# Optimization experiments

Measured on AMD Instinct MI355X. Metric: run time of the kernel, lower is better.

Reference implementation:

```python
import jax, jax.numpy as jnp
import numpy as np

N_NODES = 100000
N_EDGES = 1600000
F_IN = 128
HID = 128
LAT = 64
NUM_LAYERS = 3
NUM_GRAPHS = 512


def setup_inputs() -> dict:
    key = jax.random.key(0)
    ks = jax.random.split(key, 12)
    x = jax.random.normal(ks[0], (N_NODES, F_IN), dtype=jnp.float32)
    edge_index = jax.random.randint(ks[1], (2, N_EDGES), 0, N_NODES, dtype=jnp.int64)
    batch = jnp.sort(jax.random.randint(ks[2], (N_NODES,), 0, NUM_GRAPHS, dtype=jnp.int32))
    s_in = 1.0 / np.sqrt(F_IN)
    s_h = 1.0 / np.sqrt(HID)
    W_in = jax.random.uniform(ks[3], (F_IN, HID), jnp.float32, -s_in, s_in)
    b_in = jax.random.uniform(ks[4], (HID,), jnp.float32, -s_in, s_in)
    W_msg = jax.random.uniform(ks[5], (NUM_LAYERS, HID, HID), jnp.float32, -s_h, s_h)
    b_msg = jax.random.uniform(ks[6], (NUM_LAYERS, HID), jnp.float32, -s_h, s_h)
    W_upd = jax.random.uniform(ks[7], (NUM_LAYERS, HID, HID), jnp.float32, -s_h, s_h)
    b_upd = jax.random.uniform(ks[8], (NUM_LAYERS, HID), jnp.float32, -s_h, s_h)
    W_mean = jax.random.uniform(ks[9], (HID, LAT), jnp.float32, -s_h, s_h)
    b_mean = jax.random.uniform(ks[10], (LAT,), jnp.float32, -s_h, s_h)
    W_logvar = jax.random.uniform(ks[11], (HID, LAT), jnp.float32, -s_h, s_h)
    b_logvar = jax.random.uniform(jax.random.fold_in(key, 99), (LAT,), jnp.float32, -s_h, s_h)
    return {"x": x, "edge_index": edge_index, "batch": batch,
            "W_in": W_in, "b_in": b_in, "W_msg": W_msg, "b_msg": b_msg,
            "W_upd": W_upd, "b_upd": b_upd, "W_mean": W_mean, "b_mean": b_mean,
            "W_logvar": W_logvar, "b_logvar": b_logvar}


def _mp_layer(h, src, dst, Wm, bm, Wu, bu):
    # message: Linear+ReLU on all nodes, gather per-edge, scatter-add into dst
    messages = jax.nn.relu(h @ Wm + bm)                      # [N, H]
    agg = jax.ops.segment_sum(messages[src], dst, num_segments=N_NODES)  # [N, H]
    return jax.nn.relu(agg @ Wu + bu) + h                    # update + residual


def reference(x, edge_index, batch, W_in, b_in, W_msg, b_msg, W_upd, b_upd,
              W_mean, b_mean, W_logvar, b_logvar):
    src = edge_index[0]
    dst = edge_index[1]
    h = jax.nn.relu(x @ W_in + b_in)
    for l in range(NUM_LAYERS):
        h = _mp_layer(h, src, dst, W_msg[l], b_msg[l], W_upd[l], b_upd[l])
    # graph-level sum pooling by batch segment ids
    g = jax.ops.segment_sum(h, batch, num_segments=NUM_GRAPHS)  # [G, H]
    z_mean = g @ W_mean + b_mean
    z_logvar = g @ W_logvar + b_logvar
    return (z_mean, z_logvar)
```

## Files before the change

kernel.cpp:

```cpp
#include <hip/hip_runtime.h>
#include <hip/hip_bf16.h>
#include <cstdint>

#define N_NODES 100000
#define N_EDGES 1600000
#define N_GRAPHS 512
#define N_LAYERS 3
#define NB 1563
#define BCAP 2048
#define NFB 256

typedef __bf16 bf16x8 __attribute__((ext_vector_type(8)));
typedef float f32x4 __attribute__((ext_vector_type(4)));
typedef uint uint4v __attribute__((ext_vector_type(4)));

__device__ __forceinline__ float bf2f(ushort u) {
  uint v = ((uint)u) << 16;
  return __builtin_bit_cast(float, v);
}
__device__ __forceinline__ ushort f2bf(float f) {
  uint u = __builtin_bit_cast(uint, f);
  u += 0x7FFF + ((u >> 16) & 1);
  return (ushort)(u >> 16);
}
__device__ __forceinline__ uint pk2(float lo, float hi) {
  return (uint)f2bf(lo) | ((uint)f2bf(hi) << 16);
}

__global__ __launch_bounds__(1024) void k_bfill3(const int* __restrict__ e32,
    const long long* __restrict__ e64, int* __restrict__ bcur,
    uint* __restrict__ packed) {
  __shared__ int lcnt[NB];
  __shared__ int lbase[NB];
  __shared__ int sflag;
  const int t = threadIdx.x;
  const int e0 = blockIdx.x * (N_EDGES / NFB);
  const int e1 = e0 + (N_EDGES / NFB);
  for (int k = t; k < NB; k += 1024) lcnt[k] = 0;
  if (t == 0) {
    int any = 0;
    for (int i = 1; i < 128; i += 2) any |= e32[i];
    sflag = (any == 0) ? 1 : 0;
  }
  __syncthreads();
  const bool f64 = (sflag != 0);
  if (f64) {
    for (int i = e0 + t; i < e1; i += 1024)
      atomicAdd(&lcnt[((int)e64[N_EDGES + i]) >> 6], 1);
  } else {
    for (int i = e0 + t; i < e1; i += 1024)
      atomicAdd(&lcnt[e32[N_EDGES + i] >> 6], 1);
  }
  __syncthreads();
  for (int k = t; k < NB; k += 1024) {
    int c = lcnt[k];
    lbase[k] = (c > 0) ? atomicAdd(&bcur[k * 16], c) : 0;
    lcnt[k] = 0;
  }
  __syncthreads();
  for (int i = e0 + t; i < e1; i += 1024) {
    int d, s;
    if (f64) { d = (int)e64[N_EDGES + i]; s = (int)e64[i]; }
    else     { d = e32[N_EDGES + i];      s = e32[i]; }
    int bk = d >> 6;
    int pos = lbase[bk] + atomicAdd(&lcnt[bk], 1);
    if (pos < BCAP)
      packed[(size_t)bk * BCAP + pos] = ((uint)(d & 63) << 17) | (uint)s;
  }
}

__global__ __launch_bounds__(256) void k_bsort(const int* __restrict__ bcur,
    const uint* __restrict__ packed, uint* __restrict__ srcs,
    int* __restrict__ nbeg, int* __restrict__ nend) {
  __shared__ uint sp[BCAP];
  __shared__ uint so[BCAP];
  __shared__ int cnt[64], pref[64], cur[64];
  const int bk = blockIdx.x, t = threadIdx.x;
  const int c = min(bcur[bk * 16], BCAP);
  if (t < 64) cnt[t] = 0;
  __syncthreads();
  for (int i = t; i < c; i += 256) {
    uint p = packed[(size_t)bk * BCAP + i];
    sp[i] = p;
    atomicAdd(&cnt[p >> 17], 1);
  }
  __syncthreads();
  if (t == 0) {
    int run = 0;
    #pragma unroll
    for (int j = 0; j < 64; ++j) { pref[j] = run; run += cnt[j]; }
  }
  if (t < 64) cur[t] = 0;
  __syncthreads();
  for (int i = t; i < c; i += 256) {
    uint p = sp[i];
    int n = p >> 17;
    int pos = atomicAdd(&cur[n], 1);
    so[pref[n] + pos] = min(p & 0x1FFFF, (uint)(N_NODES - 1));
  }
  __syncthreads();
  for (int i = t; i < c; i += 256) srcs[(size_t)bk * BCAP + i] = so[i];
  if (t < 64) {
    int base = bk * BCAP;
    nbeg[bk * 64 + t] = base + pref[t];
    nend[bk * 64 + t] = base + pref[t] + cnt[t];
  }
}

__global__ __launch_bounds__(256) void k_prep_w(const float* __restrict__ W_in,
    const float* __restrict__ W_msg, const float* __restrict__ W_upd,
    ushort* __restrict__ Wt) {
  int b = blockIdx.x;
  const float* W = (b == 0) ? W_in : (b <= 3 ? W_msg + (size_t)(b - 1) * 16384
                                             : W_upd + (size_t)(b - 4) * 16384);
  ushort* O = Wt + (size_t)b * 16384;
  for (int i = threadIdx.x; i < 16384; i += 256) {
    int k = i >> 7, c = i & 127;
    O[c * 128 + k] = f2bf(W[i]);
  }
}

template <bool CVT, bool RES, bool SECOND, bool POOL>
__global__ __launch_bounds__(256) void k_gemm2(const ushort* __restrict__ Ab,
    const float* __restrict__ Af,
    const ushort* __restrict__ W1, const float* __restrict__ b1,
    const ushort* __restrict__ res, ushort* __restrict__ out1,
    const ushort* __restrict__ W2, const float* __restrict__ b2,
    ushort* __restrict__ out2,
    const int* __restrict__ batch, float* __restrict__ g) {
  __shared__ ushort sA[64][136];
  __shared__ int sb[64];
  const int t = threadIdx.x;
  const int row0 = blockIdx.x * 64;
  const int lane = t & 63;
  const int col0 = (t >> 6) * 32;
  const int lr = lane & 15, lk = (lane >> 4) * 8;

  bf16x8 bfr[4][2];
  #pragma unroll
  for (int kk = 0; kk < 4; ++kk) {
    bfr[kk][0] = *(const bf16x8*)&W1[(col0 + lr) * 128 + kk * 32 + lk];
    bfr[kk][1] = *(const bf16x8*)&W1[(col0 + 16 + lr) * 128 + kk * 32 + lk];
  }

  #pragma unroll
  for (int i = 0; i < 4; ++i) {
    int c = t + 256 * i;
    int r = c >> 4, k8 = (c & 15) * 8;
    int gr = min(row0 + r, N_NODES - 1);
    if (CVT) {
      const float* src = &Af[(size_t)gr * 128 + k8];
      float4 x0 = *(const float4*)src;
      float4 x1 = *(const float4*)(src + 4);
      uint4v u;
      u.x = pk2(x0.x, x0.y); u.y = pk2(x0.z, x0.w);
      u.z = pk2(x1.x, x1.y); u.w = pk2(x1.z, x1.w);
      *(uint4v*)&sA[r][k8] = u;
    } else {
      *(uint4*)&sA[r][k8] = *(const uint4*)&Ab[(size_t)gr * 128 + k8];
    }
  }
  __syncthreads();

  f32x4 acc[4][2] = {};
  #pragma unroll
  for (int kk = 0; kk < 4; ++kk) {
    int kb = kk * 32 + lk;
    #pragma unroll
    for (int m = 0; m < 4; ++m) {
      bf16x8 a = *(const bf16x8*)&sA[m * 16 + lr][kb];
      acc[m][0] = __builtin_amdgcn_mfma_f32_16x16x32_bf16(a, bfr[kk][0], acc[m][0], 0, 0, 0);
      acc[m][1] = __builtin_amdgcn_mfma_f32_16x16x32_bf16(a, bfr[kk][1], acc[m][1], 0, 0, 0);
    }
  }

  bf16x8 bfr2[4][2];
  if (SECOND) {
    #pragma unroll
    for (int kk = 0; kk < 4; ++kk) {
      bfr2[kk][0] = *(const bf16x8*)&W2[(col0 + lr) * 128 + kk * 32 + lk];
      bfr2[kk][1] = *(const bf16x8*)&W2[(col0 + 16 + lr) * 128 + kk * 32 + lk];
    }
  }
  __syncthreads();

  const int rb = (lane >> 4) * 4;
  #pragma unroll
  for (int n = 0; n < 2; ++n) {
    int col = col0 + n * 16 + lr;
    float bv = b1[col];
    #pragma unroll
    for (int m = 0; m < 4; ++m) {
      #pragma unroll
      for (int j = 0; j < 4; ++j) {
        int r = row0 + m * 16 + rb + j;
        float v = fmaxf(acc[m][n][j] + bv, 0.f);
        if (RES && r < N_NODES) v += bf2f(res[(size_t)r * 128 + col]);
        sA[m * 16 + rb + j][col] = f2bf(v);
      }
    }
  }
  if (POOL && t < 64)
    sb[t] = (row0 + t < N_NODES) ? batch[row0 + t] : -1;
  __syncthreads();

  if (POOL) {
    int c = t & 127, half = t >> 7;
    int v0 = half * 32, v1 = v0 + 32;
    int cur = sb[v0];
    if (cur >= 0) {
      float acc2 = 0.f;
      for (int v = v0; v < v1; ++v) {
        int b = sb[v];
        if (b < 0) break;
        if (b != cur) {
          unsafeAtomicAdd(&g[cur * 128 + c], acc2);
          acc2 = 0.f;
          cur = b;
        }
        acc2 += bf2f(sA[v][c]);
      }
      unsafeAtomicAdd(&g[cur * 128 + c], acc2);
    }
    return;
  }

  #pragma unroll
  for (int i = 0; i < 4; ++i) {
    int c = t + 256 * i;
    int r = c >> 4, k8 = (c & 15) * 8;
    int gr = row0 + r;
    if (gr < N_NODES)
      *(uint4*)&out1[(size_t)gr * 128 + k8] = *(const uint4*)&sA[r][k8];
  }

  if (SECOND) {
    f32x4 acc2[4][2] = {};
    #pragma unroll
    for (int kk = 0; kk < 4; ++kk) {
      int kb = kk * 32 + lk;
      #pragma unroll
      for (int m = 0; m < 4; ++m) {
        bf16x8 a = *(const bf16x8*)&sA[m * 16 + lr][kb];
        acc2[m][0] = __builtin_amdgcn_mfma_f32_16x16x32_bf16(a, bfr2[kk][0], acc2[m][0], 0, 0, 0);
        acc2[m][1] = __builtin_amdgcn_mfma_f32_16x16x32_bf16(a, bfr2[kk][1], acc2[m][1], 0, 0, 0);
      }
    }
    __syncthreads();

    #pragma unroll
    for (int n = 0; n < 2; ++n) {
      int col = col0 + n * 16 + lr;
      float bv = b2[col];
      #pragma unroll
      for (int m = 0; m < 4; ++m) {
        #pragma unroll
        for (int j = 0; j < 4; ++j) {
          float v = fmaxf(acc2[m][n][j] + bv, 0.f);
          sA[m * 16 + rb + j][col] = f2bf(v);
        }
      }
    }
    __syncthreads();

    #pragma unroll
    for (int i = 0; i < 4; ++i) {
      int c = t + 256 * i;
      int r = c >> 4, k8 = (c & 15) * 8;
      int gr = row0 + r;
      if (gr < N_NODES)
        *(uint4*)&out2[(size_t)gr * 128 + k8] = *(const uint4*)&sA[r][k8];
    }
  }
}

__global__ __launch_bounds__(256) void k_aggregate(const int* __restrict__ nbeg,
    const int* __restrict__ nend, const uint* __restrict__ srcs,
    const ushort* __restrict__ msg, ushort* __restrict__ agg) {
  int wid = blockIdx.x * 4 + (threadIdx.x >> 6);
  if (wid >= N_NODES) return;
  const int lane = threadIdx.x & 63;
  const uint sub = lane >> 4, l16 = lane & 15;
  int e = nbeg[wid];
  const int en = nend[wid];
  float a[8] = {0.f, 0.f, 0.f, 0.f, 0.f, 0.f, 0.f, 0.f};

#define ACC8(mv)                                              \
  a[0] += bf2f((ushort)mv.x); a[1] += bf2f((ushort)(mv.x >> 16)); \
  a[2] += bf2f((ushort)mv.y); a[3] += bf2f((ushort)(mv.y >> 16)); \
  a[4] += bf2f((ushort)mv.z); a[5] += bf2f((ushort)(mv.z >> 16)); \
  a[6] += bf2f((ushort)mv.w); a[7] += bf2f((ushort)(mv.w >> 16));

  for (; e + 16 <= en; e += 16) {
    uint s0 = srcs[e + sub];
    uint s1 = srcs[e + 4 + sub];
    uint s2 = srcs[e + 8 + sub];
    uint s3 = srcs[e + 12 + sub];
    uint4 m0 = *(const uint4*)&msg[s0 * 128u + l16 * 8u];
    uint4 m1 = *(const uint4*)&msg[s1 * 128u + l16 * 8u];
    uint4 m2 = *(const uint4*)&msg[s2 * 128u + l16 * 8u];
    uint4 m3 = *(const uint4*)&msg[s3 * 128u + l16 * 8u];
    ACC8(m0) ACC8(m1) ACC8(m2) ACC8(m3)
  }
  const uint rem = (uint)(en - e);
  #pragma unroll
  for (uint k = 0; k < 4; ++k) {
    uint idx = k * 4 + sub;
    if (idx < rem) {
      uint s = srcs[e + idx];
      uint4 m = *(const uint4*)&msg[s * 128u + l16 * 8u];
      ACC8(m)
    }
  }
#undef ACC8

  #pragma unroll
  for (int j = 0; j < 8; ++j) {
    a[j] += __shfl_xor(a[j], 16, 64);
    a[j] += __shfl_xor(a[j], 32, 64);
  }
  if (sub == 0) {
    uint4 r;
    r.x = pk2(a[0], a[1]);
    r.y = pk2(a[2], a[3]);
    r.z = pk2(a[4], a[5]);
    r.w = pk2(a[6], a[7]);
    *(uint4*)&agg[(size_t)wid * 128 + l16 * 8] = r;
  }
}

__global__ __launch_bounds__(128) void k_head(const float* __restrict__ g,
    const float* __restrict__ Wm, const float* __restrict__ bm,
    const float* __restrict__ Wl, const float* __restrict__ bl,
    float* __restrict__ out) {
  __shared__ float sg[128];
  int gr = blockIdx.x, t = threadIdx.x;
  sg[t] = g[gr * 128 + t];
  __syncthreads();
  const float* W = (t < 64) ? Wm : Wl;
  const float* b = (t < 64) ? bm : bl;
  int c = t & 63;
  float acc = b[c];
  #pragma unroll 8
  for (int k = 0; k < 128; ++k) acc += sg[k] * W[k * 64 + c];
  out[(size_t)(t < 64 ? 0 : N_GRAPHS * 64) + (size_t)gr * 64 + c] = acc;
}

extern "C" void kernel_launch(void* const* d_in, const int* in_sizes, int n_in,
                              void* d_out, int out_size, void* d_ws, size_t ws_size,
                              hipStream_t stream) {
  const float* x      = (const float*)d_in[0];
  const int* e32      = (const int*)d_in[1];
  const long long* e64 = (const long long*)d_in[1];
  const int* batch    = (const int*)d_in[2];
  const float* W_in   = (const float*)d_in[3];
  const float* b_in   = (const float*)d_in[4];
  const float* W_msg  = (const float*)d_in[5];
  const float* b_msg  = (const float*)d_in[6];
  const float* W_upd  = (const float*)d_in[7];
  const float* b_upd  = (const float*)d_in[8];
  const float* W_mean = (const float*)d_in[9];
  const float* b_mean = (const float*)d_in[10];
  const float* W_lv   = (const float*)d_in[11];
  const float* b_lv   = (const float*)d_in[12];
  float* out = (float*)d_out;

  char* p = (char*)d_ws;
  auto alloc = [&](size_t bytes) {
    char* r = p;
    p += (bytes + 255) & ~(size_t)255;
    return r;
  };
  ushort* bufA   = (ushort*)alloc((size_t)N_NODES * 128 * 2);
  ushort* bufB   = (ushort*)alloc((size_t)N_NODES * 128 * 2);
  ushort* bufC   = (ushort*)alloc((size_t)N_NODES * 128 * 2);
  ushort* bufM   = (ushort*)alloc((size_t)N_NODES * 128 * 2);
  ushort* Wt     = (ushort*)alloc((size_t)7 * 16384 * 2);
  uint*   packed = (uint*)alloc((size_t)NB * BCAP * 4);
  uint*   srcs   = (uint*)alloc((size_t)NB * BCAP * 4);
  int*    bcur   = (int*)alloc((size_t)NB * 16 * 4);
  int*    nbeg   = (int*)alloc((size_t)NB * 64 * 4);
  int*    nend   = (int*)alloc((size_t)NB * 64 * 4);
  float*  g      = (float*)alloc((size_t)N_GRAPHS * 128 * 4);

  hipMemsetAsync(bcur, 0, (size_t)NB * 16 * 4, stream);
  hipMemsetAsync(g, 0, (size_t)N_GRAPHS * 128 * 4, stream);

  k_bfill3<<<NFB, 1024, 0, stream>>>(e32, e64, bcur, packed);
  k_bsort<<<NB, 256, 0, stream>>>(bcur, packed, srcs, nbeg, nend);

  k_prep_w<<<7, 256, 0, stream>>>(W_in, W_msg, W_upd, Wt);

  const int GB = NB;
  const ushort* Wm[3] = {Wt + 16384, Wt + 2 * 16384, Wt + 3 * 16384};
  const ushort* Wu[3] = {Wt + 4 * 16384, Wt + 5 * 16384, Wt + 6 * 16384};

  k_gemm2<true, false, true, false><<<GB, 256, 0, stream>>>(
      nullptr, x, Wt, b_in, nullptr, bufA, Wm[0], b_msg, bufM, nullptr, nullptr);

  ushort* h = bufA;
  ushort* hn = bufB;
  for (int l = 0; l < N_LAYERS; ++l) {
    k_aggregate<<<(N_NODES + 3) / 4, 256, 0, stream>>>(nbeg, nend, srcs, bufM, bufC);
    if (l < N_LAYERS - 1) {
      k_gemm2<false, true, true, false><<<GB, 256, 0, stream>>>(
          bufC, nullptr, Wu[l], b_upd + (size_t)l * 128, h, hn,
          Wm[l + 1], b_msg + (size_t)(l + 1) * 128, bufM, nullptr, nullptr);
      ushort* sw = h; h = hn; hn = sw;
    } else {
      k_gemm2<false, true, false, true><<<GB, 256, 0, stream>>>(
          bufC, nullptr, Wu[l], b_upd + (size_t)l * 128, h, nullptr,
          nullptr, nullptr, nullptr, batch, g);
    }
  }

  k_head<<<N_GRAPHS, 128, 0, stream>>>(g, W_mean, b_mean, W_lv, b_lv, out);
}
```

Baseline: 389.3 us.

## Merge independent setup kernels into fewer launches with block-range dispatch

```diff
diff --git a/kernel.cpp b/kernel.cpp
--- a/kernel.cpp
+++ b/kernel.cpp
@@ -27,111 +27,62 @@
   return (uint)f2bf(lo) | ((uint)f2bf(hi) << 16);
 }
 
-__global__ __launch_bounds__(1024) void k_bfill3(const int* __restrict__ e32,
-    const long long* __restrict__ e64, int* __restrict__ bcur,
-    uint* __restrict__ packed) {
-  __shared__ int lcnt[NB];
-  __shared__ int lbase[NB];
-  __shared__ int sflag;
-  const int t = threadIdx.x;
-  const int e0 = blockIdx.x * (N_EDGES / NFB);
-  const int e1 = e0 + (N_EDGES / NFB);
-  for (int k = t; k < NB; k += 1024) lcnt[k] = 0;
-  if (t == 0) {
-    int any = 0;
-    for (int i = 1; i < 128; i += 2) any |= e32[i];
-    sflag = (any == 0) ? 1 : 0;
-  }
-  __syncthreads();
-  const bool f64 = (sflag != 0);
-  if (f64) {
-    for (int i = e0 + t; i < e1; i += 1024)
-      atomicAdd(&lcnt[((int)e64[N_EDGES + i]) >> 6], 1);
-  } else {
-    for (int i = e0 + t; i < e1; i += 1024)
-      atomicAdd(&lcnt[e32[N_EDGES + i] >> 6], 1);
-  }
-  __syncthreads();
-  for (int k = t; k < NB; k += 1024) {
-    int c = lcnt[k];
-    lbase[k] = (c > 0) ? atomicAdd(&bcur[k * 16], c) : 0;
-    lcnt[k] = 0;
-  }
-  __syncthreads();
-  for (int i = e0 + t; i < e1; i += 1024) {
-    int d, s;
-    if (f64) { d = (int)e64[N_EDGES + i]; s = (int)e64[i]; }
-    else     { d = e32[N_EDGES + i];      s = e32[i]; }
-    int bk = d >> 6;
-    int pos = lbase[bk] + atomicAdd(&lcnt[bk], 1);
-    if (pos < BCAP)
-      packed[(size_t)bk * BCAP + pos] = ((uint)(d & 63) << 17) | (uint)s;
-  }
-}
-
-__global__ __launch_bounds__(256) void k_bsort(const int* __restrict__ bcur,
-    const uint* __restrict__ packed, uint* __restrict__ srcs,
-    int* __restrict__ nbeg, int* __restrict__ nend) {
-  __shared__ uint sp[BCAP];
-  __shared__ uint so[BCAP];
-  __shared__ int cnt[64], pref[64], cur[64];
-  const int bk = blockIdx.x, t = threadIdx.x;
+struct BsortSh {
+  uint sp[BCAP];
+  uint so[BCAP];
+  int cnt[64], pref[64], cur[64];
+};
+struct GemmSh {
+  ushort sA[64][136];
+  int sb[64];
+};
+union FatSh {
+  BsortSh b;
+  GemmSh g;
+};
+
+__device__ __forceinline__ void bsort_body(BsortSh& S, int bk, int t,
+    const int* __restrict__ bcur, const uint* __restrict__ packed,
+    uint* __restrict__ srcs, int* __restrict__ nbeg, int* __restrict__ nend) {
   const int c = min(bcur[bk * 16], BCAP);
-  if (t < 64) cnt[t] = 0;
+  if (t < 64) S.cnt[t] = 0;
   __syncthreads();
   for (int i = t; i < c; i += 256) {
     uint p = packed[(size_t)bk * BCAP + i];
-    sp[i] = p;
-    atomicAdd(&cnt[p >> 17], 1);
+    S.sp[i] = p;
+    atomicAdd(&S.cnt[p >> 17], 1);
   }
   __syncthreads();
   if (t == 0) {
     int run = 0;
     #pragma unroll
-    for (int j = 0; j < 64; ++j) { pref[j] = run; run += cnt[j]; }
-  }
-  if (t < 64) cur[t] = 0;
+    for (int j = 0; j < 64; ++j) { S.pref[j] = run; run += S.cnt[j]; }
+  }
+  if (t < 64) S.cur[t] = 0;
   __syncthreads();
   for (int i = t; i < c; i += 256) {
-    uint p = sp[i];
+    uint p = S.sp[i];
     int n = p >> 17;
-    int pos = atomicAdd(&cur[n], 1);
-    so[pref[n] + pos] = min(p & 0x1FFFF, (uint)(N_NODES - 1));
-  }
-  __syncthreads();
-  for (int i = t; i < c; i += 256) srcs[(size_t)bk * BCAP + i] = so[i];
+    int pos = atomicAdd(&S.cur[n], 1);
+    S.so[S.pref[n] + pos] = min(p & 0x1FFFF, (uint)(N_NODES - 1));
+  }
+  __syncthreads();
+  for (int i = t; i < c; i += 256) srcs[(size_t)bk * BCAP + i] = S.so[i];
   if (t < 64) {
     int base = bk * BCAP;
-    nbeg[bk * 64 + t] = base + pref[t];
-    nend[bk * 64 + t] = base + pref[t] + cnt[t];
-  }
-}
-
-__global__ __launch_bounds__(256) void k_prep_w(const float* __restrict__ W_in,
-    const float* __restrict__ W_msg, const float* __restrict__ W_upd,
-    ushort* __restrict__ Wt) {
-  int b = blockIdx.x;
-  const float* W = (b == 0) ? W_in : (b <= 3 ? W_msg + (size_t)(b - 1) * 16384
-                                             : W_upd + (size_t)(b - 4) * 16384);
-  ushort* O = Wt + (size_t)b * 16384;
-  for (int i = threadIdx.x; i < 16384; i += 256) {
-    int k = i >> 7, c = i & 127;
-    O[c * 128 + k] = f2bf(W[i]);
+    nbeg[bk * 64 + t] = base + S.pref[t];
+    nend[bk * 64 + t] = base + S.pref[t] + S.cnt[t];
   }
 }
 
 template <bool CVT, bool RES, bool SECOND, bool POOL>
-__global__ __launch_bounds__(256) void k_gemm2(const ushort* __restrict__ Ab,
-    const float* __restrict__ Af,
+__device__ __forceinline__ void gemm2_body(GemmSh& S, int row0, int t,
+    const ushort* __restrict__ Ab, const float* __restrict__ Af,
     const ushort* __restrict__ W1, const float* __restrict__ b1,
     const ushort* __restrict__ res, ushort* __restrict__ out1,
     const ushort* __restrict__ W2, const float* __restrict__ b2,
     ushort* __restrict__ out2,
     const int* __restrict__ batch, float* __restrict__ g) {
-  __shared__ ushort sA[64][136];
-  __shared__ int sb[64];
-  const int t = threadIdx.x;
-  const int row0 = blockIdx.x * 64;
   const int lane = t & 63;
   const int col0 = (t >> 6) * 32;
   const int lr = lane & 15, lk = (lane >> 4) * 8;
@@ -155,9 +106,9 @@
       uint4v u;
       u.x = pk2(x0.x, x0.y); u.y = pk2(x0.z, x0.w);
       u.z = pk2(x1.x, x1.y); u.w = pk2(x1.z, x1.w);
-      *(uint4v*)&sA[r][k8] = u;
+      *(uint4v*)&S.sA[r][k8] = u;
     } else {
-      *(uint4*)&sA[r][k8] = *(const uint4*)&Ab[(size_t)gr * 128 + k8];
+      *(uint4*)&S.sA[r][k8] = *(const uint4*)&Ab[(size_t)gr * 128 + k8];
     }
   }
   __syncthreads();
@@ -168,7 +119,7 @@
     int kb = kk * 32 + lk;
     #pragma unroll
     for (int m = 0; m < 4; ++m) {
-      bf16x8 a = *(const bf16x8*)&sA[m * 16 + lr][kb];
+      bf16x8 a = *(const bf16x8*)&S.sA[m * 16 + lr][kb];
       acc[m][0] = __builtin_amdgcn_mfma_f32_16x16x32_bf16(a, bfr[kk][0], acc[m][0], 0, 0, 0);
       acc[m][1] = __builtin_amdgcn_mfma_f32_16x16x32_bf16(a, bfr[kk][1], acc[m][1], 0, 0, 0);
     }
@@ -196,29 +147,29 @@
         int r = row0 + m * 16 + rb + j;
         float v = fmaxf(acc[m][n][j] + bv, 0.f);
         if (RES && r < N_NODES) v += bf2f(res[(size_t)r * 128 + col]);
-        sA[m * 16 + rb + j][col] = f2bf(v);
+        S.sA[m * 16 + rb + j][col] = f2bf(v);
       }
     }
   }
   if (POOL && t < 64)
-    sb[t] = (row0 + t < N_NODES) ? batch[row0 + t] : -1;
+    S.sb[t] = (row0 + t < N_NODES) ? batch[row0 + t] : -1;
   __syncthreads();
 
   if (POOL) {
     int c = t & 127, half = t >> 7;
     int v0 = half * 32, v1 = v0 + 32;
-    int cur = sb[v0];
+    int cur = S.sb[v0];
     if (cur >= 0) {
       float acc2 = 0.f;
       for (int v = v0; v < v1; ++v) {
-        int b = sb[v];
+        int b = S.sb[v];
         if (b < 0) break;
         if (b != cur) {
           unsafeAtomicAdd(&g[cur * 128 + c], acc2);
           acc2 = 0.f;
           cur = b;
         }
-        acc2 += bf2f(sA[v][c]);
+        acc2 += bf2f(S.sA[v][c]);
       }
       unsafeAtomicAdd(&g[cur * 128 + c], acc2);
     }
@@ -231,7 +182,7 @@
     int r = c >> 4, k8 = (c & 15) * 8;
     int gr = row0 + r;
     if (gr < N_NODES)
-      *(uint4*)&out1[(size_t)gr * 128 + k8] = *(const uint4*)&sA[r][k8];
+      *(uint4*)&out1[(size_t)gr * 128 + k8] = *(const uint4*)&S.sA[r][k8];
   }
 
   if (SECOND) {
@@ -241,7 +192,7 @@
       int kb = kk * 32 + lk;
       #pragma unroll
       for (int m = 0; m < 4; ++m) {
-        bf16x8 a = *(const bf16x8*)&sA[m * 16 + lr][kb];
+        bf16x8 a = *(const bf16x8*)&S.sA[m * 16 + lr][kb];
         acc2[m][0] = __builtin_amdgcn_mfma_f32_16x16x32_bf16(a, bfr2[kk][0], acc2[m][0], 0, 0, 0);
         acc2[m][1] = __builtin_amdgcn_mfma_f32_16x16x32_bf16(a, bfr2[kk][1], acc2[m][1], 0, 0, 0);
       }
@@ -257,7 +208,7 @@
         #pragma unroll
         for (int j = 0; j < 4; ++j) {
           float v = fmaxf(acc2[m][n][j] + bv, 0.f);
-          sA[m * 16 + rb + j][col] = f2bf(v);
+          S.sA[m * 16 + rb + j][col] = f2bf(v);
         }
       }
     }
@@ -269,9 +220,96 @@
       int r = c >> 4, k8 = (c & 15) * 8;
       int gr = row0 + r;
       if (gr < N_NODES)
-        *(uint4*)&out2[(size_t)gr * 128 + k8] = *(const uint4*)&sA[r][k8];
-    }
-  }
+        *(uint4*)&out2[(size_t)gr * 128 + k8] = *(const uint4*)&S.sA[r][k8];
+    }
+  }
+}
+
+__global__ __launch_bounds__(1024) void k_bfill_prep(const int* __restrict__ e32,
+    const long long* __restrict__ e64, int* __restrict__ bcur,
+    uint* __restrict__ packed,
+    const float* __restrict__ W_in, const float* __restrict__ W_msg,
+    const float* __restrict__ W_upd, ushort* __restrict__ Wt) {
+  __shared__ int lcnt[NB];
+  __shared__ int lbase[NB];
+  __shared__ int sflag;
+  const int t = threadIdx.x;
+
+  if (blockIdx.x >= NFB) {
+    int b = blockIdx.x - NFB;
+    const float* W = (b == 0) ? W_in : (b <= 3 ? W_msg + (size_t)(b - 1) * 16384
+                                               : W_upd + (size_t)(b - 4) * 16384);
+    ushort* O = Wt + (size_t)b * 16384;
+    for (int i = t; i < 16384; i += 1024) {
+      int k = i >> 7, c = i & 127;
+      O[c * 128 + k] = f2bf(W[i]);
+    }
+    return;
+  }
+
+  const int e0 = blockIdx.x * (N_EDGES / NFB);
+  const int e1 = e0 + (N_EDGES / NFB);
+  for (int k = t; k < NB; k += 1024) lcnt[k] = 0;
+  if (t == 0) {
+    int any = 0;
+    for (int i = 1; i < 128; i += 2) any |= e32[i];
+    sflag = (any == 0) ? 1 : 0;
+  }
+  __syncthreads();
+  const bool f64 = (sflag != 0);
+  if (f64) {
+    for (int i = e0 + t; i < e1; i += 1024)
+      atomicAdd(&lcnt[((int)e64[N_EDGES + i]) >> 6], 1);
+  } else {
+    for (int i = e0 + t; i < e1; i += 1024)
+      atomicAdd(&lcnt[e32[N_EDGES + i] >> 6], 1);
+  }
+  __syncthreads();
+  for (int k = t; k < NB; k += 1024) {
+    int c = lcnt[k];
+    lbase[k] = (c > 0) ? atomicAdd(&bcur[k * 16], c) : 0;
+    lcnt[k] = 0;
+  }
+  __syncthreads();
+  for (int i = e0 + t; i < e1; i += 1024) {
+    int d, s;
+    if (f64) { d = (int)e64[N_EDGES + i]; s = (int)e64[i]; }
+    else     { d = e32[N_EDGES + i];      s = e32[i]; }
+    int bk = d >> 6;
+    int pos = lbase[bk] + atomicAdd(&lcnt[bk], 1);
+    if (pos < BCAP)
+      packed[(size_t)bk * BCAP + pos] = ((uint)(d & 63) << 17) | (uint)s;
+  }
+}
+
+__global__ __launch_bounds__(256) void k_bsort_gemm(const int* __restrict__ bcur,
+    const uint* __restrict__ packed, uint* __restrict__ srcs,
+    int* __restrict__ nbeg, int* __restrict__ nend,
+    const float* __restrict__ x, const ushort* __restrict__ Wt,
+    const float* __restrict__ b_in, ushort* __restrict__ h0,
+    const ushort* __restrict__ Wm0, const float* __restrict__ bm0,
+    ushort* __restrict__ msg0) {
+  __shared__ FatSh sh;
+  if (blockIdx.x < NB) {
+    bsort_body(sh.b, blockIdx.x, threadIdx.x, bcur, packed, srcs, nbeg, nend);
+  } else {
+    gemm2_body<true, false, true, false>(sh.g, (blockIdx.x - NB) * 64,
+        threadIdx.x, nullptr, x, Wt, b_in, nullptr, h0, Wm0, bm0, msg0,
+        nullptr, nullptr);
+  }
+}
+
+template <bool CVT, bool RES, bool SECOND, bool POOL>
+__global__ __launch_bounds__(256) void k_gemm2(const ushort* __restrict__ Ab,
+    const float* __restrict__ Af,
+    const ushort* __restrict__ W1, const float* __restrict__ b1,
+    const ushort* __restrict__ res, ushort* __restrict__ out1,
+    const ushort* __restrict__ W2, const float* __restrict__ b2,
+    ushort* __restrict__ out2,
+    const int* __restrict__ batch, float* __restrict__ g) {
+  __shared__ GemmSh sh;
+  gemm2_body<CVT, RES, SECOND, POOL>(sh, blockIdx.x * 64, threadIdx.x,
+      Ab, Af, W1, b1, res, out1, W2, b2, out2, batch, g);
 }
 
 __global__ __launch_bounds__(256) void k_aggregate(const int* __restrict__ nbeg,
@@ -386,29 +424,26 @@
   hipMemsetAsync(bcur, 0, (size_t)NB * 16 * 4, stream);
   hipMemsetAsync(g, 0, (size_t)N_GRAPHS * 128 * 4, stream);
 
-  k_bfill3<<<NFB, 1024, 0, stream>>>(e32, e64, bcur, packed);
-  k_bsort<<<NB, 256, 0, stream>>>(bcur, packed, srcs, nbeg, nend);
-
-  k_prep_w<<<7, 256, 0, stream>>>(W_in, W_msg, W_upd, Wt);
-
-  const int GB = NB;
   const ushort* Wm[3] = {Wt + 16384, Wt + 2 * 16384, Wt + 3 * 16384};
   const ushort* Wu[3] = {Wt + 4 * 16384, Wt + 5 * 16384, Wt + 6 * 16384};
 
-  k_gemm2<true, false, true, false><<<GB, 256, 0, stream>>>(
-      nullptr, x, Wt, b_in, nullptr, bufA, Wm[0], b_msg, bufM, nullptr, nullptr);
+  k_bfill_prep<<<NFB + 7, 1024, 0, stream>>>(e32, e64, bcur, packed,
+                                             W_in, W_msg, W_upd, Wt);
+
+  k_bsort_gemm<<<2 * NB, 256, 0, stream>>>(bcur, packed, srcs, nbeg, nend,
+                                           x, Wt, b_in, bufA, Wm[0], b_msg, bufM);
 
   ushort* h = bufA;
   ushort* hn = bufB;
   for (int l = 0; l < N_LAYERS; ++l) {
     k_aggregate<<<(N_NODES + 3) / 4, 256, 0, stream>>>(nbeg, nend, srcs, bufM, bufC);
     if (l < N_LAYERS - 1) {
-      k_gemm2<false, true, true, false><<<GB, 256, 0, stream>>>(
+      k_gemm2<false, true, true, false><<<NB, 256, 0, stream>>>(
           bufC, nullptr, Wu[l], b_upd + (size_t)l * 128, h, hn,
           Wm[l + 1], b_msg + (size_t)(l + 1) * 128, bufM, nullptr, nullptr);
       ushort* sw = h; h = hn; hn = sw;
     } else {
-      k_gemm2<false, true, false, true><<<GB, 256, 0, stream>>>(
+      k_gemm2<false, true, false, true><<<NB, 256, 0, stream>>>(
           bufC, nullptr, Wu[l], b_upd + (size_t)l * 128, h, nullptr,
           nullptr, nullptr, nullptr, batch, g);
     }
```

Result: no change. 385.2 us (median of 2 runs) (-1.1%).
